# Kernel tuning notes

Hardware: AMD Instinct MI355X
Metric: run time of the kernel (lower is better)

The kernel has to match this reference:

```python
import jax, jax.numpy as jnp
import numpy as np

N = 100000
E = 800000
IN_DIM = 128
HID = 32   # out_channels per head
HEADS = 4
OUT_DIM = 16


def _lin_init(key, fan_in, fan_out):
    k1, k2 = jax.random.split(key)
    bound = 1.0 / np.sqrt(fan_in)
    W = jax.random.uniform(k1, (fan_in, fan_out), minval=-bound, maxval=bound, dtype=jnp.float32)
    b = jax.random.uniform(k2, (fan_out,), minval=-bound, maxval=bound, dtype=jnp.float32)
    return W, b


def setup_inputs() -> dict:
    key = jax.random.key(0)
    keys = jax.random.split(key, 12)
    x = jax.random.normal(keys[0], (N, IN_DIM), dtype=jnp.float32)
    edge_index = jax.random.randint(keys[1], (2, E), 0, N, dtype=jnp.int32)
    inp = {"x": x, "edge_index": edge_index}
    in_dims = [IN_DIM, HID]
    ki = 2
    for l in range(2):
        d_in = in_dims[l]
        Wq, bq = _lin_init(keys[ki], d_in, HEADS * HID); ki += 1
        Wk, bk = _lin_init(keys[ki], d_in, HEADS * HID); ki += 1
        Wv, bv = _lin_init(keys[ki], d_in, HEADS * HID); ki += 1
        Ws, bs = _lin_init(keys[ki], d_in, HID); ki += 1
        inp.update({f"l{l}_Wq": Wq, f"l{l}_bq": bq, f"l{l}_Wk": Wk, f"l{l}_bk": bk,
                    f"l{l}_Wv": Wv, f"l{l}_bv": bv, f"l{l}_Ws": Ws, f"l{l}_bs": bs})
    Wout, bout = _lin_init(keys[ki], HID, OUT_DIM)
    inp["Wout"] = Wout
    inp["bout"] = bout
    return inp


def transformer_conv(x, src, dst, Wq, bq, Wk, bk, Wv, bv, Ws, bs):
    n = x.shape[0]
    q = (x @ Wq + bq).reshape(n, HEADS, HID)  # [N,H,C]
    k = (x @ Wk + bk).reshape(n, HEADS, HID)
    v = (x @ Wv + bv).reshape(n, HEADS, HID)
    scale = 1.0 / np.sqrt(HID)
    # per-edge attention logits over destination neighborhoods
    alpha = jnp.einsum('ehc,ehc->eh', q[dst], k[src]) * scale  # [E,H]
    m = jax.ops.segment_max(alpha, dst, num_segments=n)        # [N,H]
    p = jnp.exp(alpha - m[dst])
    s = jax.ops.segment_sum(p, dst, num_segments=n)            # [N,H]
    a = p / s[dst]                                             # [E,H]
    msg = a[:, :, None] * v[src]                               # [E,H,C]
    agg = jax.ops.segment_sum(msg, dst, num_segments=n)        # [N,H,C]
    # concat=False semantics: mean over heads, plus root/skip linear
    return agg.mean(axis=1) + (x @ Ws + bs)


def reference(x, edge_index,
              l0_Wq, l0_bq, l0_Wk, l0_bk, l0_Wv, l0_bv, l0_Ws, l0_bs,
              l1_Wq, l1_bq, l1_Wk, l1_bk, l1_Wv, l1_bv, l1_Ws, l1_bs,
              Wout, bout):
    src, dst = edge_index[0], edge_index[1]
    h = transformer_conv(x, src, dst, l0_Wq, l0_bq, l0_Wk, l0_bk, l0_Wv, l0_bv, l0_Ws, l0_bs)
    h = jax.nn.relu(h)
    h = transformer_conv(h, src, dst, l1_Wq, l1_bq, l1_Wk, l1_bk, l1_Wv, l1_bv, l1_Ws, l1_bs)
    h = jax.nn.relu(h)
    return h @ Wout + bout
```

## Files before the change

kernel.cpp:

```cpp
#include <hip/hip_runtime.h>
#include <math.h>

#define NN 100000
#define EE 800000
#define IN_DIM 128
#define HID 32
#define HEADS 4
#define QKV 128
#define COLS 416
#define QBH_W 128
#define SB_W 32
#define KV_W 256
#define OUT_DIM 16
#define NB 98
#define NTILE 26
#define NBIN 128
#define BINW 782
#define CH 2048
#define NCHUNK 391
#define QSCALE 0.25503512f

typedef __attribute__((ext_vector_type(8))) _Float16 half8;
typedef __attribute__((ext_vector_type(4))) float floatx4;

__device__ __forceinline__ unsigned short f2bf(float f) {
    unsigned int u = __float_as_uint(f);
    unsigned int r = (u + 0x7FFF + ((u >> 16) & 1)) >> 16;
    return (unsigned short)r;
}
__device__ __forceinline__ float bf2f(unsigned short h) {
    return __uint_as_float((unsigned int)h << 16);
}
__device__ __forceinline__ float bf_lo(unsigned int d) {
    return __uint_as_float(d << 16);
}
__device__ __forceinline__ float bf_hi(unsigned int d) {
    return __uint_as_float(d & 0xFFFF0000u);
}
__device__ __forceinline__ unsigned short f2h(float f) {
    _Float16 h = (_Float16)f;
    return __builtin_bit_cast(unsigned short, h);
}

__device__ __forceinline__ void pack_one(
        const float* __restrict__ Wq, const float* __restrict__ Wk,
        const float* __restrict__ Wv, const float* __restrict__ Ws,
        const float* __restrict__ bq, const float* __restrict__ bk,
        const float* __restrict__ bv, const float* __restrict__ bs,
        unsigned short* __restrict__ Wf, float* __restrict__ bp,
        int K, int idx) {
    if (idx < COLS) {
        float b;
        if (idx < 128)      b = bq[idx];
        else if (idx < 256) b = bk[idx - 128];
        else if (idx < 384) b = bv[idx - 256];
        else                b = bs[idx - 384];
        bp[idx] = b;
    }
    int nch = K >> 5;
    if (idx >= nch * NTILE * 64) return;
    int lane = idx & 63;
    int tt = (idx >> 6) % NTILE;
    int c = idx / (NTILE * 64);
    int k0 = c * 32 + (lane >> 4) * 8;
    int col = tt * 16 + (lane & 15);
    #pragma unroll
    for (int j = 0; j < 8; ++j) {
        int k = k0 + j;
        float w;
        if (col < 128)      w = Wq[(size_t)k * 128 + col];
        else if (col < 256) w = Wk[(size_t)k * 128 + (col - 128)];
        else if (col < 384) w = Wv[(size_t)k * 128 + (col - 256)];
        else                w = Ws[(size_t)k * 32 + (col - 384)];
        Wf[(size_t)idx * 8 + j] = f2h(w);
    }
}

__global__ void pack_frag2(
        const float* __restrict__ Wq0, const float* __restrict__ Wk0,
        const float* __restrict__ Wv0, const float* __restrict__ Ws0,
        const float* __restrict__ bq0, const float* __restrict__ bk0,
        const float* __restrict__ bv0, const float* __restrict__ bs0,
        const float* __restrict__ Wq1, const float* __restrict__ Wk1,
        const float* __restrict__ Wv1, const float* __restrict__ Ws1,
        const float* __restrict__ bq1, const float* __restrict__ bk1,
        const float* __restrict__ bv1, const float* __restrict__ bs1,
        unsigned short* __restrict__ Wf0, float* __restrict__ bp0,
        unsigned short* __restrict__ Wf1, float* __restrict__ bp1) {
    const int L0N = 4 * NTILE * 64;
    int gid = blockIdx.x * blockDim.x + threadIdx.x;
    if (gid < L0N) {
        pack_one(Wq0, Wk0, Wv0, Ws0, bq0, bk0, bv0, bs0, Wf0, bp0, 128, gid);
    } else {
        pack_one(Wq1, Wk1, Wv1, Ws1, bq1, bk1, bv1, bs1, Wf1, bp1, 32, gid - L0N);
    }
}

__global__ __launch_bounds__(256) void chunk_hist(
        const int* __restrict__ ei, int* __restrict__ deg,
        int* __restrict__ cmat) {
    __shared__ int cnt[NBIN];
    const int t = threadIdx.x;
    const int c = blockIdx.x;
    const int c0 = c * CH;
    const int nc = min(CH, EE - c0);
    if (t < NBIN) cnt[t] = 0;
    __syncthreads();
    for (int i = t; i < nc; i += 256) {
        int d = ei[EE + c0 + i];
        atomicAdd(&deg[d], 1);
        atomicAdd(&cnt[d / BINW], 1);
    }
    __syncthreads();
    if (t < NBIN) cmat[c * NBIN + t] = cnt[t];
}

__global__ void block_sum(const int* __restrict__ deg, int* __restrict__ partial) {
    __shared__ int sdata[256];
    int b = blockIdx.x, t = threadIdx.x;
    int sum = 0;
    for (int i = t; i < 1024; i += 256) {
        int g = b * 1024 + i;
        if (g < NN) sum += deg[g];
    }
    sdata[t] = sum; __syncthreads();
    for (int s = 128; s > 0; s >>= 1) {
        if (t < s) sdata[t] += sdata[t + s];
        __syncthreads();
    }
    if (t == 0) partial[b] = sdata[0];
}

__global__ void scan_partial(int* __restrict__ partial) {
    int l = threadIdx.x;
    int a = (l < NB) ? partial[l] : 0;
    int b = (l + 64 < NB) ? partial[l + 64] : 0;
    for (int off = 1; off < 64; off <<= 1) {
        int v = __shfl_up(a, off);
        if (l >= off) a += v;
    }
    int tot = __shfl(a, 63);
    for (int off = 1; off < 64; off <<= 1) {
        int v = __shfl_up(b, off);
        if (l >= off) b += v;
    }
    b += tot;
    int ea = __shfl_up(a, 1); if (l == 0) ea = 0;
    int eb = __shfl_up(b, 1); if (l == 0) eb = tot;
    if (l < NB) partial[l] = ea;
    if (l + 64 < NB) partial[l + 64] = eb;
}

__global__ void block_scan(const int* __restrict__ deg, const int* __restrict__ partial,
                           int* __restrict__ roff, int* __restrict__ woff) {
    __shared__ int ssum[256];
    int b = blockIdx.x, t = threadIdx.x;
    int base = b * 1024 + t * 4;
    int v[4]; int s = 0;
    #pragma unroll
    for (int i = 0; i < 4; ++i) {
        int g = base + i;
        v[i] = (g < NN) ? deg[g] : 0;
        s += v[i];
    }
    ssum[t] = s; __syncthreads();
    for (int off = 1; off < 256; off <<= 1) {
        int val = (t >= off) ? ssum[t - off] : 0;
        __syncthreads();
        ssum[t] += val;
        __syncthreads();
    }
    int excl = (t == 0) ? 0 : ssum[t - 1];
    excl += partial[b];
    #pragma unroll
    for (int i = 0; i < 4; ++i) {
        int g = base + i;
        if (g < NN) { roff[g] = excl; woff[g] = excl; }
        excl += v[i];
    }
    if (b == NB - 1 && t == 255) roff[NN] = EE;
}

__global__ void bin_offsets(const int* __restrict__ cmat, const int* __restrict__ roff,
                            int* __restrict__ omat) {
    int b = threadIdx.x;
    if (b >= NBIN) return;
    int d0 = b * BINW;
    int run = roff[d0 < NN ? d0 : NN];
    for (int c = 0; c < NCHUNK; ++c) {
        omat[c * NBIN + b] = run;
        run += cmat[c * NBIN + b];
    }
}

__global__ __launch_bounds__(256) void bin_scatter(
        const int* __restrict__ ei, const int* __restrict__ omat,
        int2* __restrict__ pairs) {
    __shared__ int cnt[NBIN], excl[NBIN], cur[NBIN], gbase[NBIN];
    __shared__ int2 stg[CH];
    __shared__ unsigned char binof[CH];
    const int t = threadIdx.x;
    const int c = blockIdx.x;
    const int c0 = c * CH;
    const int nc = min(CH, EE - c0);
    if (t < NBIN) cnt[t] = 0;
    __syncthreads();
    int msrc[8], mdst[8], mbin[8];
    #pragma unroll
    for (int i = 0; i < 8; ++i) {
        int idx = t + i * 256;
        if (idx < nc) {
            msrc[i] = ei[c0 + idx];
            mdst[i] = ei[EE + c0 + idx];
            mbin[i] = mdst[i] / BINW;
            atomicAdd(&cnt[mbin[i]], 1);
        }
    }
    __syncthreads();
    if (t < NBIN) excl[t] = cnt[t];
    __syncthreads();
    for (int off = 1; off < NBIN; off <<= 1) {
        int v = (t < NBIN && t >= off) ? excl[t - off] : 0;
        __syncthreads();
        if (t < NBIN) excl[t] += v;
        __syncthreads();
    }
    if (t < NBIN) {
        int e2 = excl[t] - cnt[t];
        excl[t] = e2; cur[t] = e2;
        gbase[t] = omat[c * NBIN + t];
    }
    __syncthreads();
    #pragma unroll
    for (int i = 0; i < 8; ++i) {
        int idx = t + i * 256;
        if (idx < nc) {
            int pos = atomicAdd(&cur[mbin[i]], 1);
            stg[pos] = make_int2(msrc[i], mdst[i]);
            binof[pos] = (unsigned char)mbin[i];
        }
    }
    __syncthreads();
    for (int i = t; i < nc; i += 256) {
        int b = binof[i];
        pairs[gbase[b] + (i - excl[b])] = stg[i];
    }
}

__global__ __launch_bounds__(256) void bin_sort(
        const int2* __restrict__ pairs, const int* __restrict__ roff,
        int* __restrict__ esrc) {
    __shared__ int cursor[BINW];
    __shared__ int loc[8192];
    const int b = blockIdx.x;
    const int t = threadIdx.x;
    const int d0 = b * BINW;
    const int d1 = (d0 + BINW < NN) ? d0 + BINW : NN;
    const int base = roff[d0];
    const int end  = roff[d1];
    const int cnt = end - base;
    for (int d = t; d < d1 - d0; d += 256) cursor[d] = roff[d0 + d] - base;
    __syncthreads();
    for (int i = t; i < cnt; i += 256) {
        int2 p = pairs[base + i];
        int pos = atomicAdd(&cursor[p.y - d0], 1);
        loc[pos] = p.x;
    }
    __syncthreads();
    for (int i = t; i < cnt; i += 256) esrc[base + i] = loc[i];
}

template <int NCH, bool F32>
__global__ __launch_bounds__(256, 3) void gemm_mfma(
        const void* __restrict__ A0,
        const unsigned short* __restrict__ Wf,
        const float* __restrict__ bp, unsigned short* __restrict__ qbh,
        float* __restrict__ sb, unsigned short* __restrict__ kvb) {
    constexpr int K = NCH * 32;
    constexpr int ROWB = 2 * K;
    constexpr int SWZ = (NCH == 4) ? 7 : 3;
    __shared__ char xlds[128 * ROWB];
    __shared__ char olds[4][32][128];
    const int tid = threadIdx.x;
    const int lane = tid & 63;
    const int wv = tid >> 6;
    const int m0b = blockIdx.x << 7;
    const int ml = lane & 15;
    const int quad = lane >> 4;

    if constexpr (F32) {
        const char* X = (const char*)A0;
        const int NPF = 128 * (K / 4);
        for (int p = tid; p < NPF; p += 256) {
            int row = p / (K / 4);
            int pc = p % (K / 4);
            int grow = m0b + row;
            if (grow >= NN) grow = NN - 1;
            float4 v = *(const float4*)(X + (size_t)grow * (4 * K) + pc * 16);
            ushort4 h = {f2h(v.x), f2h(v.y), f2h(v.z), f2h(v.w)};
            int addr = row * ROWB + ((pc * 8) ^ ((row & SWZ) << 4));
            *(ushort4*)(xlds + addr) = h;
        }
    } else {
        const char* X = (const char*)A0;
        const int NP = 128 * ROWB / 16;
        for (int p = tid; p < NP; p += 256) {
            int gb = p * 16;
            int row = gb / ROWB;
            int col = gb & (ROWB - 1);
            int grow = m0b + row;
            if (grow >= NN) grow = NN - 1;
            uint4 d = *(const uint4*)(X + (size_t)grow * ROWB + col);
            *(uint4*)(xlds + row * ROWB + (col ^ ((row & SWZ) << 4))) = d;
        }
    }
    __syncthreads();

    const int m0 = m0b + (wv << 5);
    const int rowL0 = (wv << 5) + ml;
    const int rowL1 = rowL0 + 16;
    char* myl = &olds[wv][0][0];

    for (int g = 0; g < 7; ++g) {
        int tiles[4]; int ntl = 4; int gtype;
        if (g < 2) {
            gtype = 0;
            #pragma unroll
            for (int i = 0; i < 4; ++i) tiles[i] = 4 * g + i;
        } else if (g < 6) {
            gtype = 1;
            int j = g - 2;
            tiles[0] = 8 + 2 * j; tiles[1] = 9 + 2 * j;
            tiles[2] = 16 + 2 * j; tiles[3] = 17 + 2 * j;
        } else {
            gtype = 2; ntl = 2;
            tiles[0] = 24; tiles[1] = 25; tiles[2] = 24; tiles[3] = 25;
        }

        floatx4 acc[2][4] = {};

        #pragma unroll
        for (int c = 0; c < NCH; ++c) {
            int colb = (c * 64 + quad * 16);
            int a0 = rowL0 * ROWB + (colb ^ ((rowL0 & SWZ) << 4));
            int a1 = rowL1 * ROWB + (colb ^ ((rowL1 & SWZ) << 4));
            half8 x0 = *(const half8*)(xlds + a0);
            half8 x1 = *(const half8*)(xlds + a1);
            #pragma unroll
            for (int t = 0; t < 4; ++t) {
                if (t < ntl) {
                    size_t boff = (((size_t)c * NTILE + tiles[t]) * 64 + lane) * 8;
                    half8 w = *(const half8*)(Wf + boff);
                    acc[0][t] = __builtin_amdgcn_mfma_f32_16x16x32_f16(w, x0, acc[0][t], 0, 0, 0);
                    acc[1][t] = __builtin_amdgcn_mfma_f32_16x16x32_f16(w, x1, acc[1][t], 0, 0, 0);
                }
            }
        }

        #pragma unroll
        for (int t = 0; t < 4; ++t) {
            if (t >= ntl) break;
            int tg = tiles[t];
            int c0 = (tg << 4) + (quad << 2);
            float4 b4 = *(const float4*)(bp + c0);
            #pragma unroll
            for (int mt = 0; mt < 2; ++mt) {
                int row = mt * 16 + ml;
                int sz = (row & 7) << 4;
                float v0 = acc[mt][t][0] + b4.x;
                float v1 = acc[mt][t][1] + b4.y;
                float v2 = acc[mt][t][2] + b4.z;
                float v3 = acc[mt][t][3] + b4.w;
                if (gtype == 2) {
                    *(float4*)(myl + row * 128 + ((64 * t + 16 * quad) ^ sz)) =
                        make_float4(v0, v1, v2, v3);
                } else {
                    ushort4 u = {f2bf(v0), f2bf(v1), f2bf(v2), f2bf(v3)};
                    int off;
                    if (gtype == 0) off = 32 * t + 8 * quad;
                    else off = 64 * (t & 1) + 16 * quad + 8 * (t >> 1);
                    *(ushort4*)(myl + row * 128 + (off ^ sz)) = u;
                }
            }
        }

        const int lr = lane >> 3;
        const int lc = (lane & 7) * 16;
        #pragma unroll
        for (int i = 0; i < 4; ++i) {
            int row = i * 8 + lr;
            uint4 d = *(const uint4*)(myl + row * 128 + (lc ^ (lr << 4)));
            int node = m0 + row;
            if (node < NN) {
                char* dst;
                if (gtype == 0)      dst = (char*)qbh + (size_t)node * 256 + g * 128 + lc;
                else if (gtype == 1) dst = (char*)kvb + (size_t)node * 512 + (g - 2) * 128 + lc;
                else                 dst = (char*)sb + (size_t)node * 128 + lc;
                *(uint4*)dst = d;
            }
        }
    }
}

#define ATTN_STEP(u) {                                                       \
    float k0 = bf_lo((u).x), k1 = bf_hi((u).x);                              \
    float k2 = bf_lo((u).y), k3 = bf_hi((u).y);                              \
    float v0 = bf_lo((u).z), v1 = bf_hi((u).z);                              \
    float v2 = bf_lo((u).w), v3 = bf_hi((u).w);                              \
    float part = q4.x * k0 + q4.y * k1 + q4.z * k2 + q4.w * k3;              \
    part += __shfl_xor(part, 1);                                             \
    part += __shfl_xor(part, 2);                                             \
    part += __shfl_xor(part, 4);                                             \
    float p = exp2f(part);                                                   \
    s += p;                                                                  \
    acc.x += p * v0;                                                         \
    acc.y += p * v1;                                                         \
    acc.z += p * v2;                                                         \
    acc.w += p * v3; }

__global__ __launch_bounds__(256) void fused_attn(
        const unsigned short* __restrict__ qbh, const float* __restrict__ sb,
        const unsigned short* __restrict__ kvb,
        const int* __restrict__ roff, const int* __restrict__ esrc,
        float* __restrict__ hout,
        unsigned short* __restrict__ hf) {
    const int lane = threadIdx.x & 63;
    const int w = (blockIdx.x * blockDim.x + threadIdx.x) >> 6;
    const int hw = lane >> 5;
    const int n = 2 * w + hw;
    if (n >= NN) return;
    const int kl = lane & 31;

    ushort4 qu = *(const ushort4*)(qbh + (size_t)n * QBH_W + 4 * kl);
    float4 q4 = make_float4(bf2f(qu.x) * QSCALE, bf2f(qu.y) * QSCALE,
                            bf2f(qu.z) * QSCALE, bf2f(qu.w) * QSCALE);
    float4 sk = *(const float4*)(sb + (size_t)n * SB_W + 4 * (kl & 7));

    float s = 0.f;
    float4 acc = make_float4(0.f, 0.f, 0.f, 0.f);
    const int e0 = roff[n];
    const int cnt = roff[n + 1] - e0;
    int i = 0;
    for (; i + 4 <= cnt; i += 4) {
        int b0 = esrc[e0 + i];
        int b1 = esrc[e0 + i + 1];
        int b2 = esrc[e0 + i + 2];
        int b3 = esrc[e0 + i + 3];
        uint4 u0 = *(const uint4*)(kvb + (size_t)b0 * KV_W + 8 * kl);
        uint4 u1 = *(const uint4*)(kvb + (size_t)b1 * KV_W + 8 * kl);
        uint4 u2 = *(const uint4*)(kvb + (size_t)b2 * KV_W + 8 * kl);
        uint4 u3 = *(const uint4*)(kvb + (size_t)b3 * KV_W + 8 * kl);
        ATTN_STEP(u0); ATTN_STEP(u1); ATTN_STEP(u2); ATTN_STEP(u3);
    }
    for (; i < cnt; ++i) {
        int b0 = esrc[e0 + i];
        uint4 u0 = *(const uint4*)(kvb + (size_t)b0 * KV_W + 8 * kl);
        ATTN_STEP(u0);
    }

    float inv = (s > 0.f) ? 1.f / s : 0.f;
    float4 o;
    o.x = acc.x * inv; o.y = acc.y * inv; o.z = acc.z * inv; o.w = acc.w * inv;
    o.x += __shfl_xor(o.x, 8);  o.y += __shfl_xor(o.y, 8);  o.z += __shfl_xor(o.z, 8);  o.w += __shfl_xor(o.w, 8);
    o.x += __shfl_xor(o.x, 16); o.y += __shfl_xor(o.y, 16); o.z += __shfl_xor(o.z, 16); o.w += __shfl_xor(o.w, 16);
    if (kl < 8) {
        float4 rr;
        rr.x = fmaxf(o.x * 0.25f + sk.x, 0.f);
        rr.y = fmaxf(o.y * 0.25f + sk.y, 0.f);
        rr.z = fmaxf(o.z * 0.25f + sk.z, 0.f);
        rr.w = fmaxf(o.w * 0.25f + sk.w, 0.f);
        int c0 = 4 * kl;
        if (hout)
            *(float4*)(hout + (size_t)n * HID + c0) = rr;
        if (hf) {
            ushort4 uh = {f2h(rr.x), f2h(rr.y), f2h(rr.z), f2h(rr.w)};
            *(ushort4*)(hf + (size_t)n * HID + c0) = uh;
        }
    }
}

__global__ void out_linear(const float* __restrict__ h, const float* __restrict__ Wout,
                           const float* __restrict__ bout, float* __restrict__ out) {
    int idx = blockIdx.x * blockDim.x + threadIdx.x;
    if (idx >= NN * OUT_DIM) return;
    int n = idx >> 4;
    int j = idx & 15;
    float accv = bout[j];
    #pragma unroll
    for (int k = 0; k < HID; ++k)
        accv += h[(size_t)n * HID + k] * Wout[k * OUT_DIM + j];
    out[idx] = accv;
}

extern "C" void kernel_launch(void* const* d_in, const int* in_sizes, int n_in,
                              void* d_out, int out_size, void* d_ws, size_t ws_size,
                              hipStream_t stream) {
    const float* x  = (const float*)d_in[0];
    const int*   ei = (const int*)d_in[1];
    const float* l0w[8]; const float* l1w[8];
    for (int i = 0; i < 8; ++i) { l0w[i] = (const float*)d_in[2 + i]; l1w[i] = (const float*)d_in[10 + i]; }
    const float* Wout = (const float*)d_in[18];
    const float* bout = (const float*)d_in[19];
    float* out = (float*)d_out;

    float* ws = (float*)d_ws;
    float* sb   = ws;
    float* h0   = sb + (size_t)NN * SB_W;
    float* bp0  = h0 + (size_t)NN * HID;
    float* bp1  = bp0 + COLS;
    unsigned short* qbh  = (unsigned short*)(bp1 + COLS);
    unsigned short* kvb  = qbh + (size_t)NN * QBH_W;
    unsigned short* hf   = kvb + (size_t)NN * KV_W;
    unsigned short* Wf0  = hf + (size_t)NN * HID;
    unsigned short* Wf1  = Wf0 + 4 * NTILE * 64 * 8;
    int* ibase  = (int*)(Wf1 + NTILE * 64 * 8);
    int* deg     = ibase;
    int* roff    = deg + NN;
    int* woff    = roff + NN + 1;
    int* partial = woff + NN;
    int* esrc    = partial + NB;
    int* cmat    = esrc + EE;
    int* omat    = cmat + NCHUNK * NBIN;
    int2* pairs  = (int2*)(omat + NCHUNK * NBIN);

    pack_frag2<<<(5 * NTILE * 64 + 255) / 256, 256, 0, stream>>>(
        l0w[0], l0w[2], l0w[4], l0w[6], l0w[1], l0w[3], l0w[5], l0w[7],
        l1w[0], l1w[2], l1w[4], l1w[6], l1w[1], l1w[3], l1w[5], l1w[7],
        Wf0, bp0, Wf1, bp1);

    hipMemsetAsync(deg, 0, NN * sizeof(int), stream);
    chunk_hist<<<NCHUNK, 256, 0, stream>>>(ei, deg, cmat);
    block_sum<<<NB, 256, 0, stream>>>(deg, partial);
    scan_partial<<<1, 64, 0, stream>>>(partial);
    block_scan<<<NB, 256, 0, stream>>>(deg, partial, roff, woff);
    bin_offsets<<<1, 128, 0, stream>>>(cmat, roff, omat);
    bin_scatter<<<NCHUNK, 256, 0, stream>>>(ei, omat, pairs);
    bin_sort<<<NBIN, 256, 0, stream>>>(pairs, roff, esrc);

    const int gemm_blocks = (NN + 127) / 128;
    const int attn_waves = (NN + 1) / 2;
    const int attn_blocks = (attn_waves * 64 + 255) / 256;

    gemm_mfma<4, true><<<gemm_blocks, 256, 0, stream>>>(
        x, Wf0, bp0, qbh, sb, kvb);
    fused_attn<<<attn_blocks, 256, 0, stream>>>(qbh, sb, kvb, roff, esrc,
                                                (float*)nullptr, hf);

    gemm_mfma<1, false><<<gemm_blocks, 256, 0, stream>>>(
        hf, Wf1, bp1, qbh, sb, kvb);
    fused_attn<<<attn_blocks, 256, 0, stream>>>(qbh, sb, kvb, roff, esrc, h0,
                                                (unsigned short*)nullptr);

    out_linear<<<(NN * OUT_DIM + 255) / 256, 256, 0, stream>>>(h0, Wout, bout, out);
}
```

Before: 418.5 us.

## Derive CSR offsets inside bin sort and fuse output linear into final attention

The CSR build no longer keeps global per-node degree atomics or the memset/block_sum/scan_partial/block_scan chain. Bin totals and per-chunk offsets now come from the chunk histogram through a small scan and a parallel prefix per bin. Each bin_sort block then builds its own per-node histogram and prefix to write the row offsets. Separately, the final attention kernel stages its ReLU outputs in shared memory and applies the 32x16 output linear in place, removing the h0 round trip and one launch. The cost is extra shared-memory scans and a block-wide barrier in the final attention kernel.

```diff
diff --git a/kernel.cpp b/kernel.cpp
--- a/kernel.cpp
+++ b/kernel.cpp
@@ -12,7 +12,6 @@
 #define SB_W 32
 #define KV_W 256
 #define OUT_DIM 16
-#define NB 98
 #define NTILE 26
 #define NBIN 128
 #define BINW 782
@@ -96,9 +95,9 @@
     }
 }
 
+
 __global__ __launch_bounds__(256) void chunk_hist(
-        const int* __restrict__ ei, int* __restrict__ deg,
-        int* __restrict__ cmat) {
+        const int* __restrict__ ei, int* __restrict__ cmat) {
     __shared__ int cnt[NBIN];
     const int t = threadIdx.x;
     const int c = blockIdx.x;
@@ -106,91 +105,51 @@
     const int nc = min(CH, EE - c0);
     if (t < NBIN) cnt[t] = 0;
     __syncthreads();
-    for (int i = t; i < nc; i += 256) {
-        int d = ei[EE + c0 + i];
-        atomicAdd(&deg[d], 1);
-        atomicAdd(&cnt[d / BINW], 1);
-    }
+    for (int i = t; i < nc; i += 256)
+        atomicAdd(&cnt[ei[EE + c0 + i] / BINW], 1);
     __syncthreads();
     if (t < NBIN) cmat[c * NBIN + t] = cnt[t];
 }
 
-__global__ void block_sum(const int* __restrict__ deg, int* __restrict__ partial) {
-    __shared__ int sdata[256];
-    int b = blockIdx.x, t = threadIdx.x;
-    int sum = 0;
-    for (int i = t; i < 1024; i += 256) {
-        int g = b * 1024 + i;
-        if (g < NN) sum += deg[g];
-    }
-    sdata[t] = sum; __syncthreads();
-    for (int s = 128; s > 0; s >>= 1) {
-        if (t < s) sdata[t] += sdata[t + s];
-        __syncthreads();
-    }
-    if (t == 0) partial[b] = sdata[0];
-}
-
-__global__ void scan_partial(int* __restrict__ partial) {
-    int l = threadIdx.x;
-    int a = (l < NB) ? partial[l] : 0;
-    int b = (l + 64 < NB) ? partial[l + 64] : 0;
-    for (int off = 1; off < 64; off <<= 1) {
-        int v = __shfl_up(a, off);
-        if (l >= off) a += v;
-    }
-    int tot = __shfl(a, 63);
-    for (int off = 1; off < 64; off <<= 1) {
-        int v = __shfl_up(b, off);
-        if (l >= off) b += v;
-    }
-    b += tot;
-    int ea = __shfl_up(a, 1); if (l == 0) ea = 0;
-    int eb = __shfl_up(b, 1); if (l == 0) eb = tot;
-    if (l < NB) partial[l] = ea;
-    if (l + 64 < NB) partial[l + 64] = eb;
-}
-
-__global__ void block_scan(const int* __restrict__ deg, const int* __restrict__ partial,
-                           int* __restrict__ roff, int* __restrict__ woff) {
+__global__ void btot_scan(const int* __restrict__ cmat, int* __restrict__ bbase) {
+    __shared__ int sc[NBIN];
+    int b = threadIdx.x;
+    int s = 0;
+    for (int c = 0; c < NCHUNK; ++c) s += cmat[c * NBIN + b];
+    sc[b] = s;
+    __syncthreads();
+    for (int off = 1; off < NBIN; off <<= 1) {
+        int v = (b >= off) ? sc[b - off] : 0;
+        __syncthreads();
+        sc[b] += v;
+        __syncthreads();
+    }
+    bbase[b] = sc[b] - s;
+    if (b == NBIN - 1) bbase[NBIN] = sc[NBIN - 1];
+}
+
+__global__ __launch_bounds__(256) void bin_prefix(
+        const int* __restrict__ cmat, const int* __restrict__ bbase,
+        int* __restrict__ omat) {
     __shared__ int ssum[256];
-    int b = blockIdx.x, t = threadIdx.x;
-    int base = b * 1024 + t * 4;
-    int v[4]; int s = 0;
-    #pragma unroll
-    for (int i = 0; i < 4; ++i) {
-        int g = base + i;
-        v[i] = (g < NN) ? deg[g] : 0;
-        s += v[i];
-    }
-    ssum[t] = s; __syncthreads();
+    const int b = blockIdx.x;
+    const int t = threadIdx.x;
+    const int bb = bbase[b];
+    int c0 = 2 * t;
+    int v0 = (c0 < NCHUNK) ? cmat[(size_t)c0 * NBIN + b] : 0;
+    int v1 = (c0 + 1 < NCHUNK) ? cmat[(size_t)(c0 + 1) * NBIN + b] : 0;
+    int s = v0 + v1;
+    ssum[t] = s;
+    __syncthreads();
     for (int off = 1; off < 256; off <<= 1) {
-        int val = (t >= off) ? ssum[t - off] : 0;
-        __syncthreads();
-        ssum[t] += val;
-        __syncthreads();
-    }
-    int excl = (t == 0) ? 0 : ssum[t - 1];
-    excl += partial[b];
-    #pragma unroll
-    for (int i = 0; i < 4; ++i) {
-        int g = base + i;
-        if (g < NN) { roff[g] = excl; woff[g] = excl; }
-        excl += v[i];
-    }
-    if (b == NB - 1 && t == 255) roff[NN] = EE;
-}
-
-__global__ void bin_offsets(const int* __restrict__ cmat, const int* __restrict__ roff,
-                            int* __restrict__ omat) {
-    int b = threadIdx.x;
-    if (b >= NBIN) return;
-    int d0 = b * BINW;
-    int run = roff[d0 < NN ? d0 : NN];
-    for (int c = 0; c < NCHUNK; ++c) {
-        omat[c * NBIN + b] = run;
-        run += cmat[c * NBIN + b];
-    }
+        int v = (t >= off) ? ssum[t - off] : 0;
+        __syncthreads();
+        ssum[t] += v;
+        __syncthreads();
+    }
+    int excl = ssum[t] - s;
+    if (c0 < NCHUNK) omat[(size_t)c0 * NBIN + b] = bb + excl;
+    if (c0 + 1 < NCHUNK) omat[(size_t)(c0 + 1) * NBIN + b] = bb + excl + v0;
 }
 
 __global__ __launch_bounds__(256) void bin_scatter(
@@ -248,22 +207,53 @@
 }
 
 __global__ __launch_bounds__(256) void bin_sort(
-        const int2* __restrict__ pairs, const int* __restrict__ roff,
-        int* __restrict__ esrc) {
-    __shared__ int cursor[BINW];
+        const int2* __restrict__ pairs, const int* __restrict__ bbase,
+        int* __restrict__ roff, int* __restrict__ esrc) {
+    __shared__ int hist[BINW + 2];
+    __shared__ int ssum[256];
     __shared__ int loc[8192];
     const int b = blockIdx.x;
     const int t = threadIdx.x;
     const int d0 = b * BINW;
-    const int d1 = (d0 + BINW < NN) ? d0 + BINW : NN;
-    const int base = roff[d0];
-    const int end  = roff[d1];
-    const int cnt = end - base;
-    for (int d = t; d < d1 - d0; d += 256) cursor[d] = roff[d0 + d] - base;
+    const int nd = (d0 + BINW < NN) ? BINW : (NN - d0);
+    const int base = bbase[b];
+    const int cnt = bbase[b + 1] - base;
+    for (int d = t; d < nd; d += 256) hist[d] = 0;
+    __syncthreads();
+    for (int i = t; i < cnt; i += 256)
+        atomicAdd(&hist[pairs[base + i].y - d0], 1);
+    __syncthreads();
+    int bi = t * 4;
+    int v[4]; int s = 0;
+    #pragma unroll
+    for (int i = 0; i < 4; ++i) {
+        int idx = bi + i;
+        v[i] = (idx < nd) ? hist[idx] : 0;
+        s += v[i];
+    }
+    ssum[t] = s;
+    __syncthreads();
+    for (int off = 1; off < 256; off <<= 1) {
+        int val = (t >= off) ? ssum[t - off] : 0;
+        __syncthreads();
+        ssum[t] += val;
+        __syncthreads();
+    }
+    int run = ssum[t] - s;
+    #pragma unroll
+    for (int i = 0; i < 4; ++i) {
+        int idx = bi + i;
+        if (idx < nd) {
+            hist[idx] = run;
+            roff[d0 + idx] = base + run;
+            run += v[i];
+        }
+    }
+    if (b == NBIN - 1 && t == 0) roff[NN] = EE;
     __syncthreads();
     for (int i = t; i < cnt; i += 256) {
         int2 p = pairs[base + i];
-        int pos = atomicAdd(&cursor[p.y - d0], 1);
+        int pos = atomicAdd(&hist[p.y - d0], 1);
         loc[pos] = p.x;
     }
     __syncthreads();
@@ -418,17 +408,21 @@
     acc.z += p * v2;                                                         \
     acc.w += p * v3; }
 
+template <bool FINAL>
 __global__ __launch_bounds__(256) void fused_attn(
         const unsigned short* __restrict__ qbh, const float* __restrict__ sb,
         const unsigned short* __restrict__ kvb,
         const int* __restrict__ roff, const int* __restrict__ esrc,
-        float* __restrict__ hout,
-        unsigned short* __restrict__ hf) {
-    const int lane = threadIdx.x & 63;
-    const int w = (blockIdx.x * blockDim.x + threadIdx.x) >> 6;
+        unsigned short* __restrict__ hf,
+        const float* __restrict__ Wout, const float* __restrict__ bout,
+        float* __restrict__ outp) {
+    __shared__ float hbuf[8][32];
+    const int tid = threadIdx.x;
+    const int lane = tid & 63;
+    const int w = (blockIdx.x * blockDim.x + tid) >> 6;
     const int hw = lane >> 5;
     const int n = 2 * w + hw;
-    if (n >= NN) return;
+    if (n < NN) {
     const int kl = lane & 31;
 
     ushort4 qu = *(const ushort4*)(qbh + (size_t)n * QBH_W + 4 * kl);
@@ -470,26 +464,30 @@
         rr.z = fmaxf(o.z * 0.25f + sk.z, 0.f);
         rr.w = fmaxf(o.w * 0.25f + sk.w, 0.f);
         int c0 = 4 * kl;
-        if (hout)
-            *(float4*)(hout + (size_t)n * HID + c0) = rr;
-        if (hf) {
+        if constexpr (FINAL) {
+            int slot = (tid >> 6) * 2 + hw;
+            *(float4*)(&hbuf[slot][c0]) = rr;
+        } else {
             ushort4 uh = {f2h(rr.x), f2h(rr.y), f2h(rr.z), f2h(rr.w)};
             *(ushort4*)(hf + (size_t)n * HID + c0) = uh;
         }
     }
-}
-
-__global__ void out_linear(const float* __restrict__ h, const float* __restrict__ Wout,
-                           const float* __restrict__ bout, float* __restrict__ out) {
-    int idx = blockIdx.x * blockDim.x + threadIdx.x;
-    if (idx >= NN * OUT_DIM) return;
-    int n = idx >> 4;
-    int j = idx & 15;
-    float accv = bout[j];
-    #pragma unroll
-    for (int k = 0; k < HID; ++k)
-        accv += h[(size_t)n * HID + k] * Wout[k * OUT_DIM + j];
-    out[idx] = accv;
+    }
+    if constexpr (FINAL) {
+        __syncthreads();
+        if (tid < 128) {
+            int slot = tid >> 4;
+            int j = tid & 15;
+            int n2 = blockIdx.x * 8 + slot;
+            if (n2 < NN) {
+                float a = bout[j];
+                #pragma unroll
+                for (int k = 0; k < HID; ++k)
+                    a += hbuf[slot][k] * Wout[k * OUT_DIM + j];
+                outp[(size_t)n2 * OUT_DIM + j] = a;
+            }
+        }
+    }
 }
 
 extern "C" void kernel_launch(void* const* d_in, const int* in_sizes, int n_in,
@@ -505,8 +503,7 @@
 
     float* ws = (float*)d_ws;
     float* sb   = ws;
-    float* h0   = sb + (size_t)NN * SB_W;
-    float* bp0  = h0 + (size_t)NN * HID;
+    float* bp0  = sb + (size_t)NN * SB_W;
     float* bp1  = bp0 + COLS;
     unsigned short* qbh  = (unsigned short*)(bp1 + COLS);
     unsigned short* kvb  = qbh + (size_t)NN * QBH_W;
@@ -514,28 +511,23 @@
     unsigned short* Wf0  = hf + (size_t)NN * HID;
     unsigned short* Wf1  = Wf0 + 4 * NTILE * 64 * 8;
     int* ibase  = (int*)(Wf1 + NTILE * 64 * 8);
-    int* deg     = ibase;
-    int* roff    = deg + NN;
-    int* woff    = roff + NN + 1;
-    int* partial = woff + NN;
-    int* esrc    = partial + NB;
+    int* roff    = ibase;
+    int* esrc    = roff + NN + 1;
     int* cmat    = esrc + EE;
     int* omat    = cmat + NCHUNK * NBIN;
-    int2* pairs  = (int2*)(omat + NCHUNK * NBIN);
+    int* bbase   = omat + NCHUNK * NBIN;
+    int2* pairs  = (int2*)(bbase + NBIN + 2);
 
     pack_frag2<<<(5 * NTILE * 64 + 255) / 256, 256, 0, stream>>>(
         l0w[0], l0w[2], l0w[4], l0w[6], l0w[1], l0w[3], l0w[5], l0w[7],
         l1w[0], l1w[2], l1w[4], l1w[6], l1w[1], l1w[3], l1w[5], l1w[7],
         Wf0, bp0, Wf1, bp1);
 
-    hipMemsetAsync(deg, 0, NN * sizeof(int), stream);
-    chunk_hist<<<NCHUNK, 256, 0, stream>>>(ei, deg, cmat);
-    block_sum<<<NB, 256, 0, stream>>>(deg, partial);
-    scan_partial<<<1, 64, 0, stream>>>(partial);
-    block_scan<<<NB, 256, 0, stream>>>(deg, partial, roff, woff);
-    bin_offsets<<<1, 128, 0, stream>>>(cmat, roff, omat);
+    chunk_hist<<<NCHUNK, 256, 0, stream>>>(ei, cmat);
+    btot_scan<<<1, NBIN, 0, stream>>>(cmat, bbase);
+    bin_prefix<<<NBIN, 256, 0, stream>>>(cmat, bbase, omat);
     bin_scatter<<<NCHUNK, 256, 0, stream>>>(ei, omat, pairs);
-    bin_sort<<<NBIN, 256, 0, stream>>>(pairs, roff, esrc);
+    bin_sort<<<NBIN, 256, 0, stream>>>(pairs, bbase, roff, esrc);
 
     const int gemm_blocks = (NN + 127) / 128;
     const int attn_waves = (NN + 1) / 2;
@@ -543,13 +535,12 @@
 
     gemm_mfma<4, true><<<gemm_blocks, 256, 0, stream>>>(
         x, Wf0, bp0, qbh, sb, kvb);
-    fused_attn<<<attn_blocks, 256, 0, stream>>>(qbh, sb, kvb, roff, esrc,
-                                                (float*)nullptr, hf);
+    fused_attn<false><<<attn_blocks, 256, 0, stream>>>(
+        qbh, sb, kvb, roff, esrc, hf, (const float*)nullptr,
+        (const float*)nullptr, (float*)nullptr);
 
     gemm_mfma<1, false><<<gemm_blocks, 256, 0, stream>>>(
         hf, Wf1, bp1, qbh, sb, kvb);
-    fused_attn<<<attn_blocks, 256, 0, stream>>>(qbh, sb, kvb, roff, esrc, h0,
-                                                (unsigned short*)nullptr);
-
-    out_linear<<<(NN * OUT_DIM + 255) / 256, 256, 0, stream>>>(h0, Wout, bout, out);
-}
+    fused_attn<true><<<attn_blocks, 256, 0, stream>>>(
+        qbh, sb, kvb, roff, esrc, (unsigned short*)nullptr, Wout, bout, out);
+}
```

Result: faster. 357.4 us (-14.6%).
